# Kernel optimization log

Measured on AMD Instinct MI355X. Metric: run time of the kernel, lower is better.

## Reference

```python
import jax, jax.numpy as jnp
import numpy as np
from jax import lax

B, CI, CO, H, W = 32, 64, 64, 128, 128
NUM_EXPERTS = 5
NUM_TASKS = 10  # num_tasks=9 + 1 internal global task
K = 5


def setup_inputs() -> dict:
    key = jax.random.key(0)
    ks = jax.random.split(key, 9)
    # kaiming_uniform_ with a=sqrt(5), fan_out -> bound = sqrt(6/((1+5)*fan_out))
    def kaiming(k, co, ci, ksz):
        fan_out = co * ksz * ksz
        bound = np.sqrt(6.0 / (6.0 * fan_out))
        return jax.random.uniform(k, (co, ci, ksz, ksz), jnp.float32, -bound, bound)
    gw_bound = 1.0 / np.sqrt(NUM_TASKS)
    return {
        "x": jax.random.normal(ks[0], (B, CI, H, W), jnp.float32),
        "task_id": jax.random.randint(ks[1], (B,), 0, NUM_TASKS),
        "gate_w": jax.random.uniform(ks[2], (NUM_EXPERTS * CO, NUM_TASKS), jnp.float32, -gw_bound, gw_bound),
        "gate_b": jax.random.uniform(ks[3], (NUM_EXPERTS * CO,), jnp.float32, -gw_bound, gw_bound),
        "w5": kaiming(ks[4], CO, CI, 5),
        "w3": kaiming(ks[5], CO, CI, 3),
        "w1": kaiming(ks[6], CO, CI, 1),
        "wavg3": kaiming(ks[7], CO, CI, 1),
        "wavg5": kaiming(ks[8], CO, CI, 1),
    }


def _expert_bank(w5, w3, w1, wavg3, wavg5):
    # All experts expressed as 5x5 kernels, stacked: [E, O, I, 5, 5]
    pad = lambda w, p: jnp.pad(w, ((0, 0), (0, 0), (p, p), (p, p)))
    avg3 = jnp.full((3, 3), 1.0 / 9.0, w5.dtype)
    avg5 = jnp.full((5, 5), 1.0 / 25.0, w5.dtype)
    e_conv5 = w5
    e_conv3 = pad(w3, 1)
    e_conv1 = pad(w1, 2)
    e_avg3 = pad(wavg3 * avg3[None, None], 1)  # [O,I,1,1]*[3,3] broadcast
    e_avg5 = wavg5 * avg5[None, None]
    return jnp.stack([e_conv5, e_conv3, e_conv1, e_avg3, e_avg5])


def reference(x, task_id, gate_w, gate_b, w5, w3, w1, wavg3, wavg5):
    # Gate: one-hot task -> per-(expert, out_channel) routing weights
    t = jax.nn.one_hot(task_id, NUM_TASKS, dtype=x.dtype)          # [B, T]
    g = t @ gate_w.T + gate_b                                       # [B, E*O]
    g = jax.nn.softmax(g.reshape(-1, NUM_EXPERTS, CO), axis=1)      # [B, E, O]

    experts = _expert_bank(w5, w3, w1, wavg3, wavg5)                # [E, O, I, 5, 5]
    # Batched kernel synthesis (replaces per-sample python loop of einsums)
    w = jnp.einsum('eoikl,beo->boikl', experts, g)                  # [B, O, I, 5, 5]

    # Per-sample conv2d, stride 1, 'same' padding
    def conv1(xi, wi):
        return lax.conv_general_dilated(
            xi[None], wi, (1, 1), 'SAME',
            dimension_numbers=('NCHW', 'OIHW', 'NCHW'))[0]
    y = jax.vmap(conv1)(x, w)                                       # [B, O, H, W]
    # conv_type='final' -> Identity subsequent layer; eval mode -> task_id unchanged
    return y, task_id
```

## Files before the change

### kernel.cpp

```cpp
#include <hip/hip_runtime.h>

#define WK_OFFSET_BYTES 71368704ull

using bf16x8   = __attribute__((ext_vector_type(8)))  __bf16;
using floatx16 = __attribute__((ext_vector_type(16))) float;

static __device__ __forceinline__ unsigned short f2bf(float f) {
    unsigned int u = __float_as_uint(f);
    u += 0x7FFFu + ((u >> 16) & 1u);
    return (unsigned short)(u >> 16);
}

static __device__ __forceinline__ floatx16 mfma16(bf16x8 a, bf16x8 b, floatx16 c) {
    return __builtin_amdgcn_mfma_f32_32x32x16_bf16(a, b, c, 0, 0, 0);
}

static __device__ __forceinline__ void gload_lds16(const void* g, void* l) {
    __builtin_amdgcn_global_load_lds(
        (const __attribute__((address_space(1))) void*)g,
        (__attribute__((address_space(3))) void*)l, 16, 0, 0);
}

__global__ __launch_bounds__(256) void pre_kernel(
    const float* __restrict__ x,
    const float* __restrict__ gate_w, const float* __restrict__ gate_b,
    const float* __restrict__ w5, const float* __restrict__ w3,
    const float* __restrict__ w1, const float* __restrict__ wavg3,
    const float* __restrict__ wavg5, const int* __restrict__ task_id,
    unsigned short* __restrict__ xt, unsigned short* __restrict__ wk,
    float* __restrict__ out_task)
{
    const int blk = blockIdx.x;
    const int tid = threadIdx.x;
    __shared__ float g[5][64];

    if (blk < 4224) {
        const int b  = blk / 132;
        const int hp = blk - b * 132;
        const int h  = hp - 2;
        const bool vrow = (h >= 0) && (h < 128);
        unsigned short* dst_row = xt + (size_t)blk * 8448;

        for (int i = tid; i < 1056; i += 256) {
            int cc = i / 132;
            int wp = i - cc * 132;
            unsigned int pk[4] = {0u, 0u, 0u, 0u};
            if (vrow && wp >= 2 && wp < 130) {
                const float* xp = x + (((size_t)(b * 64 + cc * 8) * 128 + h) * 128 + (wp - 2));
                #pragma unroll
                for (int j = 0; j < 4; ++j) {
                    unsigned short lo = f2bf(xp[(2 * j)     * 16384]);
                    unsigned short hi = f2bf(xp[(2 * j + 1) * 16384]);
                    pk[j] = (unsigned int)lo | ((unsigned int)hi << 16);
                }
            }
            *(uint4*)(dst_row + (size_t)i * 8) = make_uint4(pk[0], pk[1], pk[2], pk[3]);
        }
    } else {
        const int pb = blk - 4224;
        const int t = pb >> 4;
        const int chunk = pb & 15;

        if (tid < 64) {
            float l[5];
            float m = -1e30f;
            #pragma unroll
            for (int e = 0; e < 5; ++e) {
                l[e] = gate_w[(e * 64 + tid) * 10 + t] + gate_b[e * 64 + tid];
                m = fmaxf(m, l[e]);
            }
            float s = 0.f;
            #pragma unroll
            for (int e = 0; e < 5; ++e) { l[e] = expf(l[e] - m); s += l[e]; }
            float inv = 1.f / s;
            #pragma unroll
            for (int e = 0; e < 5; ++e) g[e][tid] = l[e] * inv;
        }
        __syncthreads();

        for (int it = 0; it < 25; ++it) {
            int idx = chunk * 6400 + it * 256 + tid;
            int ci  = idx & 63;
            int o   = (idx >> 6) & 63;
            int tap = idx >> 12;
            int ky = tap / 5, kx = tap - ky * 5;

            float v = g[0][o] * w5[(o * 64 + ci) * 25 + tap];
            bool in3 = (ky >= 1 && ky <= 3 && kx >= 1 && kx <= 3);
            if (in3) {
                v += g[1][o] * w3[(o * 64 + ci) * 9 + (ky - 1) * 3 + (kx - 1)];
                v += g[3][o] * wavg3[o * 64 + ci] * (1.f / 9.f);
            }
            if (ky == 2 && kx == 2) v += g[2][o] * w1[o * 64 + ci];
            v += g[4][o] * wavg5[o * 64 + ci] * (1.f / 25.f);

            wk[(t * 25 + tap) * 4096 + o * 64 + ci] = f2bf(v);
        }

        if (pb == 0 && tid < 32) out_task[tid] = (float)task_id[tid];
    }
}

__global__ __launch_bounds__(512, 2) void conv_kernel(
    const unsigned short* __restrict__ xt, const unsigned short* __restrict__ wk,
    const int* __restrict__ task_id, float* __restrict__ out)
{
    __shared__ unsigned short ibuf[2][25344];
    __shared__ unsigned short wlds[25600];

    const int blk = ((blockIdx.x & 7) << 6) | (blockIdx.x >> 3);
    const int b  = blk >> 4;
    const int ht = blk & 15;
    const int t  = task_id[b];

    const int tid  = threadIdx.x;
    const int lane = tid & 63;
    const int wave = tid >> 6;
    const int lane31 = lane & 31;
    const int laneh  = lane >> 5;

    floatx16 acc[2][4];
    #pragma unroll
    for (int c = 0; c < 2; ++c)
        #pragma unroll
        for (int p = 0; p < 4; ++p)
            #pragma unroll
            for (int r = 0; r < 16; ++r) acc[c][p][r] = 0.f;

    const unsigned short* wkt = wk + t * 102400;
    const size_t ibase0 = ((size_t)(b * 132 + ht * 8)) * 8448;

    auto stage_i = [&](int s, int q) {
        const unsigned short* gsrc = xt + ibase0 + q * 2112;
        unsigned short* ldst = &ibuf[s][0];
        #pragma unroll
        for (int j = 0; j < 6; ++j) {
            int i = j * 512 + tid;
            int r = i / 264;
            int rem = i - r * 264;
            gload_lds16(gsrc + (size_t)r * 8448 + rem * 8, ldst + i * 8);
        }
        if (tid < 96) {
            int i = 3072 + tid;
            int r = i / 264;
            int rem = i - r * 264;
            gload_lds16(gsrc + (size_t)r * 8448 + rem * 8, ldst + i * 8);
        }
    };
    auto stage_w = [&](int q) {
        const unsigned short* gsrc = wkt + q * 16;
        unsigned short* ldst = &wlds[0];
        #pragma unroll
        for (int j = 0; j < 6; ++j) {
            int i = j * 512 + tid;
            int tap = i >> 7;
            int rem = i & 127;
            int cih = rem >> 6;
            int co  = rem & 63;
            gload_lds16(gsrc + tap * 4096 + co * 64 + cih * 8, ldst + i * 8);
        }
        if (tid < 128) {
            int i = 3072 + tid;
            int tap = i >> 7;
            int rem = i & 127;
            int cih = rem >> 6;
            int co  = rem & 63;
            gload_lds16(gsrc + tap * 4096 + co * 64 + cih * 8, ldst + i * 8);
        }
    };

    stage_w(0);
    stage_i(0, 0);
    asm volatile("s_waitcnt vmcnt(0)" ::: "memory");
    __builtin_amdgcn_s_barrier();
    __builtin_amdgcn_sched_barrier(0);

    for (int q = 0; q < 4; ++q) {
        const int s = q & 1;
        if (q < 3) stage_i(s ^ 1, q + 1);

        const unsigned short* ib = &ibuf[s][0];
        __builtin_amdgcn_s_setprio(1);
        #pragma unroll
        for (int ky = 0; ky < 5; ++ky) {
            const unsigned short* lrow = ib + (wave + ky) * 2112 + laneh * 1056;
            const unsigned short* wrow = wlds + (ky * 5) * 1024 + laneh * 512 + lane31 * 8;
            #pragma unroll
            for (int kx = 0; kx < 5; ++kx) {
                const unsigned short* ap = wrow + kx * 1024;
                bf16x8 a0 = *(const bf16x8*)(ap);
                bf16x8 a1 = *(const bf16x8*)(ap + 256);

                bf16x8 bb[4];
                #pragma unroll
                for (int p = 0; p < 4; ++p)
                    bb[p] = *(const bf16x8*)(lrow + (p * 32 + lane31 + kx) * 8);

                #pragma unroll
                for (int p = 0; p < 4; ++p) {
                    acc[0][p] = mfma16(a0, bb[p], acc[0][p]);
                    acc[1][p] = mfma16(a1, bb[p], acc[1][p]);
                }
            }
        }
        __builtin_amdgcn_s_setprio(0);

        asm volatile("s_waitcnt lgkmcnt(0)" ::: "memory");
        __builtin_amdgcn_s_barrier();
        __builtin_amdgcn_sched_barrier(0);
        if (q < 3) {
            stage_w(q + 1);
            asm volatile("s_waitcnt vmcnt(0)" ::: "memory");
            __builtin_amdgcn_s_barrier();
            __builtin_amdgcn_sched_barrier(0);
        }
    }

    const int h = ht * 8 + wave;
    #pragma unroll
    for (int c = 0; c < 2; ++c) {
        #pragma unroll
        for (int p = 0; p < 4; ++p) {
            int w = p * 32 + lane31;
            #pragma unroll
            for (int reg = 0; reg < 16; ++reg) {
                int co = c * 32 + (reg & 3) + 8 * (reg >> 2) + 4 * laneh;
                out[((size_t)(b * 64 + co) * 128 + h) * 128 + w] = acc[c][p][reg];
            }
        }
    }
}

extern "C" void kernel_launch(void* const* d_in, const int* in_sizes, int n_in,
                              void* d_out, int out_size, void* d_ws, size_t ws_size,
                              hipStream_t stream) {
    const float* x       = (const float*)d_in[0];
    const int*   task_id = (const int*)  d_in[1];
    const float* gate_w  = (const float*)d_in[2];
    const float* gate_b  = (const float*)d_in[3];
    const float* w5      = (const float*)d_in[4];
    const float* w3      = (const float*)d_in[5];
    const float* w1      = (const float*)d_in[6];
    const float* wavg3   = (const float*)d_in[7];
    const float* wavg5   = (const float*)d_in[8];

    float* out = (float*)d_out;
    float* out_task = out + 32 * 64 * 128 * 128;

    unsigned short* xt = (unsigned short*)d_ws;
    unsigned short* wk = (unsigned short*)((char*)d_ws + WK_OFFSET_BYTES);

    pre_kernel<<<dim3(4384), dim3(256), 0, stream>>>(
        x, gate_w, gate_b, w5, w3, w1, wavg3, wavg5, task_id, xt, wk, out_task);
    conv_kernel<<<dim3(512), dim3(512), 0, stream>>>(xt, wk, task_id, out);
}
```

Baseline: 351.9 us.

## Remap waves to 4-row by 32-column tiles and reuse input rows across ky taps

Each wave's output tile changes from one row by 128 columns to four rows by 32 columns. Weight fragments for all five ky taps are held in registers per kx, and each loaded input row feeds several output rows. This reduces LDS reads of input (8 row loads per kx instead of 20) and reuses the weight fragments across rows. In exchange it keeps 10 weight fragments live in registers, which adds register pressure under launch bounds of 512 threads with 2 blocks per CU. It also changes the output store pattern to 32-column segments.

```diff
diff --git a/kernel.cpp b/kernel.cpp
--- a/kernel.cpp
+++ b/kernel.cpp
@@ -116,16 +116,18 @@
     const int tid  = threadIdx.x;
     const int lane = tid & 63;
     const int wave = tid >> 6;
+    const int rg = wave >> 2;
+    const int wc = wave & 3;
     const int lane31 = lane & 31;
     const int laneh  = lane >> 5;
 
-    floatx16 acc[2][4];
+    floatx16 acc[4][2];
     #pragma unroll
-    for (int c = 0; c < 2; ++c)
-        #pragma unroll
-        for (int p = 0; p < 4; ++p)
-            #pragma unroll
-            for (int r = 0; r < 16; ++r) acc[c][p][r] = 0.f;
+    for (int o = 0; o < 4; ++o)
+        #pragma unroll
+        for (int c = 0; c < 2; ++c)
+            #pragma unroll
+            for (int r = 0; r < 16; ++r) acc[o][c][r] = 0.f;
 
     const unsigned short* wkt = wk + t * 102400;
     const size_t ibase0 = ((size_t)(b * 132 + ht * 8)) * 8448;
@@ -182,24 +184,28 @@
         const unsigned short* ib = &ibuf[s][0];
         __builtin_amdgcn_s_setprio(1);
         #pragma unroll
-        for (int ky = 0; ky < 5; ++ky) {
-            const unsigned short* lrow = ib + (wave + ky) * 2112 + laneh * 1056;
-            const unsigned short* wrow = wlds + (ky * 5) * 1024 + laneh * 512 + lane31 * 8;
-            #pragma unroll
-            for (int kx = 0; kx < 5; ++kx) {
-                const unsigned short* ap = wrow + kx * 1024;
-                bf16x8 a0 = *(const bf16x8*)(ap);
-                bf16x8 a1 = *(const bf16x8*)(ap + 256);
-
-                bf16x8 bb[4];
+        for (int kx = 0; kx < 5; ++kx) {
+            bf16x8 aF[5][2];
+            #pragma unroll
+            for (int ky = 0; ky < 5; ++ky) {
+                const unsigned short* ap =
+                    wlds + (ky * 5 + kx) * 1024 + laneh * 512 + lane31 * 8;
+                aF[ky][0] = *(const bf16x8*)(ap);
+                aF[ky][1] = *(const bf16x8*)(ap + 256);
+            }
+            #pragma unroll
+            for (int hr = 0; hr < 8; ++hr) {
+                const unsigned short* bp =
+                    ib + (rg * 4 + hr) * 2112 + laneh * 1056
+                       + (wc * 32 + lane31 + kx) * 8;
+                bf16x8 bb = *(const bf16x8*)bp;
                 #pragma unroll
-                for (int p = 0; p < 4; ++p)
-                    bb[p] = *(const bf16x8*)(lrow + (p * 32 + lane31 + kx) * 8);
-
-                #pragma unroll
-                for (int p = 0; p < 4; ++p) {
-                    acc[0][p] = mfma16(a0, bb[p], acc[0][p]);
-                    acc[1][p] = mfma16(a1, bb[p], acc[1][p]);
+                for (int ky = 0; ky < 5; ++ky) {
+                    const int o = hr - ky;
+                    if (o >= 0 && o < 4) {
+                        acc[o][0] = mfma16(aF[ky][0], bb, acc[o][0]);
+                        acc[o][1] = mfma16(aF[ky][1], bb, acc[o][1]);
+                    }
                 }
             }
         }
@@ -216,16 +222,16 @@
         }
     }
 
-    const int h = ht * 8 + wave;
     #pragma unroll
-    for (int c = 0; c < 2; ++c) {
-        #pragma unroll
-        for (int p = 0; p < 4; ++p) {
-            int w = p * 32 + lane31;
+    for (int o = 0; o < 4; ++o) {
+        const int h = ht * 8 + rg * 4 + o;
+        #pragma unroll
+        for (int c = 0; c < 2; ++c) {
+            const int w = wc * 32 + lane31;
             #pragma unroll
             for (int reg = 0; reg < 16; ++reg) {
                 int co = c * 32 + (reg & 3) + 8 * (reg >> 2) + 4 * laneh;
-                out[((size_t)(b * 64 + co) * 128 + h) * 128 + w] = acc[c][p][reg];
+                out[((size_t)(b * 64 + co) * 128 + h) * 128 + w] = acc[o][c][reg];
             }
         }
     }
```

New measurement: 351.0 us. No clear change (-0.3%).
